# Kernel tuning notes

Measured on AMD Instinct MI355X. Metric: run time of the kernel, lower is better.

The kernel has to match this reference:

```python
import jax, jax.numpy as jnp
import numpy as np

DIM = 4096
N_HEADS = 32
HEAD_DIM = 128
N_KV = 8
REP = N_HEADS // N_KV  # 4
B = 8       # number of packed sequences (block-diagonal blocks)
S = 1024    # tokens per sequence
T = B * S   # seqlen_sum = 8192


def setup_inputs() -> dict:
    key = jax.random.key(0)
    ks = jax.random.split(key, 6)
    x = jax.random.normal(ks[0], (T, DIM), dtype=jnp.float32)
    # RoPE freqs: positions restart at 0 for each packed sequence
    pos = jnp.tile(jnp.arange(S, dtype=jnp.float32), B)            # [T]
    inv_freq = 1.0 / (10000.0 ** (jnp.arange(0, HEAD_DIM, 2, dtype=jnp.float32) / HEAD_DIM))  # [HEAD_DIM//2]
    freqs = pos[:, None] * inv_freq[None, :]                       # [T, HEAD_DIM//2]
    cos = jnp.cos(freqs)
    sin = jnp.sin(freqs)
    s = 0.02
    wq = jax.random.normal(ks[1], (DIM, N_HEADS * HEAD_DIM), dtype=jnp.float32) * s
    wk = jax.random.normal(ks[2], (DIM, N_KV * HEAD_DIM), dtype=jnp.float32) * s
    wv = jax.random.normal(ks[3], (DIM, N_KV * HEAD_DIM), dtype=jnp.float32) * s
    wo = jax.random.normal(ks[4], (N_HEADS * HEAD_DIM, DIM), dtype=jnp.float32) * s
    return {"x": x, "cos": cos, "sin": sin, "wq": wq, "wk": wk, "wv": wv, "wo": wo}


def _rope(t, cos, sin):
    # t: [T, H, D]; cos/sin: [T, D//2]; complex rotation on (even, odd) pairs
    th, hd = t.shape[1], t.shape[2]
    tp = t.reshape(t.shape[0], th, hd // 2, 2)
    te, to = tp[..., 0], tp[..., 1]
    c = cos[:, None, :]
    s = sin[:, None, :]
    oe = te * c - to * s
    oo = te * s + to * c
    return jnp.stack([oe, oo], axis=-1).reshape(t.shape)


def reference(x, cos, sin, wq, wk, wv, wo):
    scale = HEAD_DIM ** -0.5
    q = (x @ wq).reshape(T, N_HEADS, HEAD_DIM)
    k = (x @ wk).reshape(T, N_KV, HEAD_DIM)
    v = (x @ wv).reshape(T, N_KV, HEAD_DIM)
    q = _rope(q, cos, sin)
    k = _rope(k, cos, sin)
    # Block-diagonal mask with equal blocks == batched attention over B sequences.
    # GQA: q head index h = kv*REP + r (matches repeat_interleave on kv dim),
    # so group q heads as [N_KV, REP] instead of materializing repeated K/V.
    q = q.reshape(B, S, N_KV, REP, HEAD_DIM)
    k = k.reshape(B, S, N_KV, HEAD_DIM)
    v = v.reshape(B, S, N_KV, HEAD_DIM)
    scores = jnp.einsum('bqkrd,bskd->bkrqs', q, k) * scale   # [B, N_KV, REP, S, S]
    attn = jax.nn.softmax(scores, axis=-1)
    out = jnp.einsum('bkrqs,bskd->bqkrd', attn, v)           # [B, S, N_KV, REP, D]
    out = out.reshape(T, N_HEADS * HEAD_DIM)
    return out @ wo
```

## Files before the change

kernel.cpp:

```cpp
#include <hip/hip_runtime.h>
#include <math.h>

typedef unsigned short ushort_t;
typedef __attribute__((ext_vector_type(8))) short short8;
typedef __attribute__((ext_vector_type(4))) float f32x4;

#define MFMA16(a, b, c) __builtin_amdgcn_mfma_f32_16x16x32_bf16(a, b, c, 0, 0, 0)

__device__ __forceinline__ ushort_t f2bf(float f) {
    union { float f; unsigned u; } v;
    v.f = f;
    unsigned r = v.u + 0x7FFF + ((v.u >> 16) & 1);
    return (ushort_t)(r >> 16);
}

__device__ __forceinline__ void gload_lds16(const ushort_t* g, ushort_t* l) {
    __builtin_amdgcn_global_load_lds(
        (const __attribute__((address_space(1))) void*)g,
        (__attribute__((address_space(3))) void*)l, 16, 0, 0);
}

__global__ __launch_bounds__(256) void cast_f32_bf16(const float* __restrict__ src,
                                                     ushort_t* __restrict__ dst, int n8) {
    int i = blockIdx.x * 256 + threadIdx.x;
    if (i >= n8) return;
    const float4* s = (const float4*)src;
    float4 a = s[2 * i], b = s[2 * i + 1];
    union { ushort_t u[8]; uint4 v; } o;
    o.u[0] = f2bf(a.x); o.u[1] = f2bf(a.y); o.u[2] = f2bf(a.z); o.u[3] = f2bf(a.w);
    o.u[4] = f2bf(b.x); o.u[5] = f2bf(b.y); o.u[6] = f2bf(b.z); o.u[7] = f2bf(b.w);
    ((uint4*)dst)[i] = o.v;
}

__global__ __launch_bounds__(256) void transpose_cast(const float* __restrict__ src,
                                                      int D, int N,
                                                      ushort_t* __restrict__ dst, int dstStride) {
    __shared__ float t[32][33];
    int n0 = blockIdx.x * 32, d0 = blockIdx.y * 32;
    int tx = threadIdx.x & 31, ty = threadIdx.x >> 5;
#pragma unroll
    for (int i = 0; i < 4; i++)
        t[ty + 8 * i][tx] = src[(size_t)(d0 + ty + 8 * i) * N + n0 + tx];
    __syncthreads();
#pragma unroll
    for (int i = 0; i < 4; i++) {
        int n = ty + 8 * i;
        dst[(size_t)(n0 + n) * dstStride + d0 + tx] = f2bf(t[tx][n]);
    }
}

__global__ __launch_bounds__(256) void transpose_v(const ushort_t* __restrict__ qkv,
                                                   ushort_t* __restrict__ vt) {
    __shared__ ushort_t t[32][33];
    int bk = blockIdx.z; int b = bk >> 3, kvh = bk & 7;
    int s0 = blockIdx.x * 32, d0 = blockIdx.y * 32;
    int tx = threadIdx.x & 31, ty = threadIdx.x >> 5;
#pragma unroll
    for (int i = 0; i < 4; i++)
        t[ty + 8 * i][tx] = qkv[(size_t)(b * 1024 + s0 + ty + 8 * i) * 6144 + 5120 + kvh * 128 + d0 + tx];
    __syncthreads();
#pragma unroll
    for (int i = 0; i < 4; i++)
        vt[((size_t)(b * 8 + kvh) * 128 + d0 + ty + 8 * i) * 1024 + s0 + tx] = t[tx][ty + 8 * i];
}

template <int EPI>
__global__ __launch_bounds__(512, 2) void gemm8x(
    const ushort_t* __restrict__ A, const ushort_t* __restrict__ Bt,
    ushort_t* __restrict__ obf, float* __restrict__ of32,
    int M, int N, int K,
    const float* __restrict__ cosT, const float* __restrict__ sinT) {
    extern __shared__ __align__(16) ushort_t lds[];
    const int tid = threadIdx.x;
    const int lane = tid & 63, wv = tid >> 6;
    const int wr = wv >> 2, wc = wv & 3;
    const int lr = lane & 15, g = lane >> 4;

    const int gx = gridDim.x;
    const int nwg = gx * gridDim.y;
    const int bid = blockIdx.y * gx + blockIdx.x;
    const int swz = (bid & 7) * (nwg >> 3) + (bid >> 3);
    const int brow = (swz / gx) * 256, bcol = (swz % gx) * 256;

    const int st_r = tid >> 3, st_p = tid & 7;
    const int cA = (st_p ^ (st_r & 7)) * 8;
    const size_t aS0 = (size_t)(brow + st_r) * K + cA;
    const size_t bS0 = (size_t)(bcol + st_r) * K + cA;
    const int dstT = st_r * 64 + st_p * 8;

    const int sl0 = (g ^ (lr & 7)) * 8;
    const int sl1 = ((4 + g) ^ (lr & 7)) * 8;
    const int aRow = (wr * 128 + lr) * 64;
    const int bRow = (wc * 64 + lr) * 64;

    f32x4 acc[8][4];
#pragma unroll
    for (int m = 0; m < 8; m++)
#pragma unroll
        for (int n = 0; n < 4; n++) acc[m][n] = (f32x4){0.f, 0.f, 0.f, 0.f};

#define STG_A(kn, roff)                                                          \
    gload_lds16(A + aS0 + (size_t)(roff) * K + (size_t)(kn) * 64,                \
                lds + ((kn) & 1) * 16384 + (roff) * 64 + dstT)
#define STG_B(kn, roff)                                                          \
    gload_lds16(Bt + bS0 + (size_t)(roff) * K + (size_t)(kn) * 64,               \
                lds + 32768 + ((kn) & 1) * 16384 + (roff) * 64 + dstT)

    STG_B(0, 0);  STG_B(0, 64);
    STG_B(0, 128); STG_B(0, 192);
    STG_A(0, 0);  STG_A(0, 128);
    STG_A(0, 64); STG_A(0, 192);

    const int NKT = K >> 6;
    for (int kt = 0; kt < NKT; ++kt) {
        const int buf = (kt & 1) * 16384;
        const bool stg = kt < NKT - 1;
        const int kn = kt + 1;
        short8 bfr[4], af[4];

        asm volatile("s_waitcnt vmcnt(2)" ::: "memory");
        __builtin_amdgcn_s_barrier();
        __builtin_amdgcn_sched_barrier(0);
#pragma unroll
        for (int n = 0; n < 4; ++n)
            bfr[n] = *(const short8*)(lds + 32768 + buf + bRow + n * 1024 + sl0);
#pragma unroll
        for (int m = 0; m < 4; ++m)
            af[m] = *(const short8*)(lds + buf + aRow + m * 1024 + sl0);
        if (stg) { STG_B(kn, 0); STG_B(kn, 64); }
        __builtin_amdgcn_sched_barrier(0);
        __builtin_amdgcn_s_setprio(1);
#pragma unroll
        for (int m = 0; m < 4; ++m)
#pragma unroll
            for (int n = 0; n < 4; ++n)
                acc[m][n] = MFMA16(af[m], bfr[n], acc[m][n]);
        __builtin_amdgcn_s_setprio(0);

        if (kt == NKT - 1) asm volatile("s_waitcnt vmcnt(0)" ::: "memory");
        else               asm volatile("s_waitcnt vmcnt(2)" ::: "memory");
        __builtin_amdgcn_s_barrier();
        __builtin_amdgcn_sched_barrier(0);
#pragma unroll
        for (int m = 0; m < 4; ++m)
            af[m] = *(const short8*)(lds + buf + aRow + 4096 + m * 1024 + sl0);
        if (stg) { STG_B(kn, 128); STG_B(kn, 192); }
        __builtin_amdgcn_sched_barrier(0);
        __builtin_amdgcn_s_setprio(1);
#pragma unroll
        for (int m = 0; m < 4; ++m)
#pragma unroll
            for (int n = 0; n < 4; ++n)
                acc[m + 4][n] = MFMA16(af[m], bfr[n], acc[m + 4][n]);
        __builtin_amdgcn_s_setprio(0);

        __builtin_amdgcn_s_barrier();
        __builtin_amdgcn_sched_barrier(0);
#pragma unroll
        for (int n = 0; n < 4; ++n)
            bfr[n] = *(const short8*)(lds + 32768 + buf + bRow + n * 1024 + sl1);
#pragma unroll
        for (int m = 0; m < 4; ++m)
            af[m] = *(const short8*)(lds + buf + aRow + m * 1024 + sl1);
        if (stg) { STG_A(kn, 0); STG_A(kn, 128); }
        __builtin_amdgcn_sched_barrier(0);
        __builtin_amdgcn_s_setprio(1);
#pragma unroll
        for (int m = 0; m < 4; ++m)
#pragma unroll
            for (int n = 0; n < 4; ++n)
                acc[m][n] = MFMA16(af[m], bfr[n], acc[m][n]);
        __builtin_amdgcn_s_setprio(0);

        __builtin_amdgcn_s_barrier();
        __builtin_amdgcn_sched_barrier(0);
#pragma unroll
        for (int m = 0; m < 4; ++m)
            af[m] = *(const short8*)(lds + buf + aRow + 4096 + m * 1024 + sl1);
        if (stg) { STG_A(kn, 64); STG_A(kn, 192); }
        __builtin_amdgcn_sched_barrier(0);
        __builtin_amdgcn_s_setprio(1);
#pragma unroll
        for (int m = 0; m < 4; ++m)
#pragma unroll
            for (int n = 0; n < 4; ++n)
                acc[m + 4][n] = MFMA16(af[m], bfr[n], acc[m + 4][n]);
        __builtin_amdgcn_s_setprio(0);
    }
#undef STG_A
#undef STG_B

#pragma unroll
    for (int m = 0; m < 8; ++m) {
#pragma unroll
        for (int n = 0; n < 4; ++n) {
#pragma unroll
            for (int reg = 0; reg < 4; ++reg) {
                int r = brow + wr * 128 + m * 16 + g * 4 + reg;
                int c = bcol + wc * 64 + n * 16 + lr;
                float val = acc[m][n][reg];
                if (EPI == 1) {
                    float other = __shfl_xor(val, 1, 64);
                    if (c < 5120) {
                        int pos = r & 1023;
                        int pair = (c & 127) >> 1;
                        float cz = cosT[pos * 64 + pair];
                        float sz = sinT[pos * 64 + pair];
                        val = val * cz + other * ((c & 1) ? sz : -sz);
                        if (c < 4096) val *= 0.12752551286084110f;
                    }
                    obf[(size_t)r * N + c] = f2bf(val);
                } else {
                    of32[(size_t)r * N + c] = val;
                }
            }
        }
    }
}

__global__ __launch_bounds__(512, 2) void attn_fwd2(const ushort_t* __restrict__ qkv,
                                                    const ushort_t* __restrict__ vt,
                                                    ushort_t* __restrict__ aout) {
    extern __shared__ __align__(16) ushort_t lds[];
    const int tid = threadIdx.x, lane = tid & 63, w = tid >> 6;
    const int lr = lane & 15, g = lane >> 4;
    const int hr = w & 3, qc = w >> 2;
    const int qt = blockIdx.x, kvh = blockIdx.y, b = blockIdx.z;
    const int h = kvh * 4 + hr;
    const size_t qRow0 = (size_t)b * 1024 + qt * 64 + qc * 32;
    const size_t kBase = (size_t)b * 1024 * 6144 + 4096 + kvh * 128;
    const size_t vBase = (size_t)(b * 8 + kvh) * 128 * 1024;
    ushort_t* Pw = lds + 32768 + w * 2304;

    short8 qf[2][4];
#pragma unroll
    for (int qg = 0; qg < 2; ++qg)
#pragma unroll
        for (int kd = 0; kd < 4; ++kd)
            qf[qg][kd] = *(const short8*)&qkv[(qRow0 + qg * 16 + lr) * 6144 + h * 128 + kd * 32 + g * 8];

    f32x4 o[2][8];
#pragma unroll
    for (int qg = 0; qg < 2; ++qg)
#pragma unroll
        for (int nd = 0; nd < 8; ++nd) o[qg][nd] = (f32x4){0.f, 0.f, 0.f, 0.f};
    f32x4 lsum[2];
    lsum[0] = (f32x4){0.f, 0.f, 0.f, 0.f};
    lsum[1] = (f32x4){0.f, 0.f, 0.f, 0.f};

#define STAGE_KV(kt)                                                                   \
    {                                                                                  \
        const int buf_ = (kt) & 1;                                                     \
        {                                                                              \
            const int r0_ = tid >> 4, p_ = tid & 15;                                   \
            gload_lds16(qkv + kBase + (size_t)((kt) * 64 + r0_) * 6144 + ((p_ ^ (r0_ & 7)) * 8), \
                        lds + buf_ * 8192 + r0_ * 128 + p_ * 8);                       \
            const int r1_ = r0_ + 32;                                                  \
            gload_lds16(qkv + kBase + (size_t)((kt) * 64 + r1_) * 6144 + ((p_ ^ (r1_ & 7)) * 8), \
                        lds + buf_ * 8192 + r1_ * 128 + p_ * 8);                       \
        }                                                                              \
        {                                                                              \
            const int d0_ = tid >> 3, p_ = tid & 7;                                    \
            gload_lds16(vt + vBase + (size_t)d0_ * 1024 + (kt) * 64 + ((p_ ^ (d0_ & 7)) * 8), \
                        lds + 16384 + buf_ * 8192 + d0_ * 64 + p_ * 8);                \
            const int d1_ = d0_ + 64;                                                  \
            gload_lds16(vt + vBase + (size_t)d1_ * 1024 + (kt) * 64 + ((p_ ^ (d1_ & 7)) * 8), \
                        lds + 16384 + buf_ * 8192 + d1_ * 64 + p_ * 8);                \
        }                                                                              \
    }

    STAGE_KV(0);

    for (int kt = 0; kt < 16; ++kt) {
        const int buf = kt & 1;
        if (kt < 15) {
            STAGE_KV(kt + 1);
            asm volatile("s_waitcnt vmcnt(4)" ::: "memory");
        } else {
            asm volatile("s_waitcnt vmcnt(0)" ::: "memory");
        }
        __builtin_amdgcn_s_barrier();

        f32x4 sc[2][4];
#pragma unroll
        for (int qg = 0; qg < 2; ++qg)
#pragma unroll
            for (int ns = 0; ns < 4; ++ns) sc[qg][ns] = (f32x4){0.f, 0.f, 0.f, 0.f};
        __builtin_amdgcn_s_setprio(1);
#pragma unroll
        for (int ns = 0; ns < 4; ++ns) {
            const int key = ns * 16 + lr;
#pragma unroll
            for (int kd = 0; kd < 4; ++kd) {
                const short8 kf = *(const short8*)(lds + buf * 8192 + key * 128 +
                                                   (((kd * 4 + g) ^ (lr & 7)) * 8));
                sc[0][ns] = MFMA16(qf[0][kd], kf, sc[0][ns]);
                sc[1][ns] = MFMA16(qf[1][kd], kf, sc[1][ns]);
            }
        }
        __builtin_amdgcn_s_setprio(0);

#pragma unroll
        for (int qg = 0; qg < 2; ++qg) {
#pragma unroll
            for (int ns = 0; ns < 4; ++ns) {
#pragma unroll
                for (int j = 0; j < 4; ++j) {
                    float p = exp2f(sc[qg][ns][j]);
                    sc[qg][ns][j] = p;
                    lsum[qg][j] += p;
                }
            }
        }
#pragma unroll
        for (int qg = 0; qg < 2; ++qg)
#pragma unroll
            for (int ns = 0; ns < 4; ++ns)
#pragma unroll
                for (int j = 0; j < 4; ++j)
                    Pw[(qg * 16 + g * 4 + j) * 72 + ns * 16 + lr] = f2bf(sc[qg][ns][j]);

        __builtin_amdgcn_s_setprio(1);
#pragma unroll
        for (int ks = 0; ks < 2; ++ks) {
            short8 pa[2];
            pa[0] = *(const short8*)(Pw + (0 + lr) * 72 + ks * 32 + g * 8);
            pa[1] = *(const short8*)(Pw + (16 + lr) * 72 + ks * 32 + g * 8);
#pragma unroll
            for (int nd = 0; nd < 8; ++nd) {
                const int d = nd * 16 + lr;
                const short8 vf = *(const short8*)(lds + 16384 + buf * 8192 + d * 64 +
                                                   (((ks * 4 + g) ^ (d & 7)) * 8));
                o[0][nd] = MFMA16(pa[0], vf, o[0][nd]);
                o[1][nd] = MFMA16(pa[1], vf, o[1][nd]);
            }
        }
        __builtin_amdgcn_s_setprio(0);
        __builtin_amdgcn_s_barrier();
    }
#undef STAGE_KV

#pragma unroll
    for (int qg = 0; qg < 2; ++qg) {
#pragma unroll
        for (int j = 0; j < 4; ++j) {
            float s = lsum[qg][j];
            s += __shfl_xor(s, 1, 64);
            s += __shfl_xor(s, 2, 64);
            s += __shfl_xor(s, 4, 64);
            s += __shfl_xor(s, 8, 64);
            const float inv = 1.0f / s;
            const size_t r = qRow0 + qg * 16 + g * 4 + j;
#pragma unroll
            for (int nd = 0; nd < 8; ++nd)
                aout[r * 4096 + h * 128 + nd * 16 + lr] = f2bf(o[qg][nd][j] * inv);
        }
    }
}

extern "C" void kernel_launch(void* const* d_in, const int* in_sizes, int n_in,
                              void* d_out, int out_size, void* d_ws, size_t ws_size,
                              hipStream_t stream) {
    const float* x    = (const float*)d_in[0];
    const float* cosT = (const float*)d_in[1];
    const float* sinT = (const float*)d_in[2];
    const float* wq   = (const float*)d_in[3];
    const float* wk   = (const float*)d_in[4];
    const float* wv   = (const float*)d_in[5];
    const float* wo   = (const float*)d_in[6];
    float* out = (float*)d_out;

    char* ws = (char*)d_ws;
    ushort_t* xb   = (ushort_t*)(ws);
    ushort_t* wT   = (ushort_t*)(ws + 67108864);
    ushort_t* woT  = (ushort_t*)(ws + 117440512);
    ushort_t* qkv  = (ushort_t*)(ws + 150994944);
    ushort_t* vtb  = (ushort_t*)(ws + 67108864);
    ushort_t* attn = (ushort_t*)(ws);

    hipFuncSetAttribute((const void*)gemm8x<1>, hipFuncAttributeMaxDynamicSharedMemorySize, 131072);
    hipFuncSetAttribute((const void*)gemm8x<2>, hipFuncAttributeMaxDynamicSharedMemorySize, 131072);
    hipFuncSetAttribute((const void*)attn_fwd2, hipFuncAttributeMaxDynamicSharedMemorySize, 102400);

    cast_f32_bf16<<<16384, 256, 0, stream>>>(x, xb, 8192 * 4096 / 8);
    transpose_cast<<<dim3(128, 128), 256, 0, stream>>>(wq, 4096, 4096, wT, 4096);
    transpose_cast<<<dim3(32, 128), 256, 0, stream>>>(wk, 4096, 1024, wT + (size_t)4096 * 4096, 4096);
    transpose_cast<<<dim3(32, 128), 256, 0, stream>>>(wv, 4096, 1024, wT + (size_t)5120 * 4096, 4096);
    transpose_cast<<<dim3(128, 128), 256, 0, stream>>>(wo, 4096, 4096, woT, 4096);

    gemm8x<1><<<dim3(24, 32), 512, 131072, stream>>>(xb, wT, qkv, nullptr, 8192, 6144, 4096, cosT, sinT);
    transpose_v<<<dim3(32, 4, 64), 256, 0, stream>>>(qkv, vtb);
    attn_fwd2<<<dim3(16, 8, 8), 512, 102400, stream>>>(qkv, vtb, attn);
    gemm8x<2><<<dim3(16, 32), 512, 131072, stream>>>(attn, woT, nullptr, out, 8192, 4096, 4096, nullptr, nullptr);
}
```

Measured before the change: 940.8 us.

## Triple-buffer A tiles in GEMM LDS pipeline with two-stage-ahead prefetch

Restructures the bf16 GEMM main loop so A tiles are triple-buffered in LDS and prefetched two K-steps ahead, while B stays double-buffered. Waits and barriers are reorganized: a single vmcnt wait per iteration, explicit lgkmcnt waits before each MFMA block, and extra barriers around each LDS read phase. The aim is to hide more global-load latency behind MFMA work. In exchange, dynamic LDS grows to 160KB, which fills the whole LDS per CU, and the added barriers could add synchronization stalls.

```diff
diff --git a/kernel.cpp b/kernel.cpp
--- a/kernel.cpp
+++ b/kernel.cpp
@@ -65,7 +65,7 @@
 }
 
 template <int EPI>
-__global__ __launch_bounds__(512, 2) void gemm8x(
+__global__ __launch_bounds__(512, 2) void gemm9(
     const ushort_t* __restrict__ A, const ushort_t* __restrict__ Bt,
     ushort_t* __restrict__ obf, float* __restrict__ of32,
     int M, int N, int K,
@@ -101,33 +101,34 @@
 
 #define STG_A(kn, roff)                                                          \
     gload_lds16(A + aS0 + (size_t)(roff) * K + (size_t)(kn) * 64,                \
-                lds + ((kn) & 1) * 16384 + (roff) * 64 + dstT)
+                lds + ((kn) % 3) * 16384 + (roff) * 64 + dstT)
 #define STG_B(kn, roff)                                                          \
     gload_lds16(Bt + bS0 + (size_t)(roff) * K + (size_t)(kn) * 64,               \
-                lds + 32768 + ((kn) & 1) * 16384 + (roff) * 64 + dstT)
-
-    STG_B(0, 0);  STG_B(0, 64);
-    STG_B(0, 128); STG_B(0, 192);
-    STG_A(0, 0);  STG_A(0, 128);
-    STG_A(0, 64); STG_A(0, 192);
+                lds + 49152 + ((kn) & 1) * 16384 + (roff) * 64 + dstT)
+
+    STG_A(0, 0); STG_A(0, 64); STG_A(0, 128); STG_A(0, 192);
+    STG_B(0, 0); STG_B(0, 64); STG_B(0, 128); STG_B(0, 192);
+    STG_A(1, 0); STG_A(1, 64); STG_A(1, 128); STG_A(1, 192);
+    asm volatile("s_waitcnt vmcnt(4)" ::: "memory");
+    __builtin_amdgcn_s_barrier();
 
     const int NKT = K >> 6;
     for (int kt = 0; kt < NKT; ++kt) {
-        const int buf = (kt & 1) * 16384;
-        const bool stg = kt < NKT - 1;
-        const int kn = kt + 1;
+        const int sa = (kt % 3) * 16384;
+        const int sb = 49152 + (kt & 1) * 16384;
+        const bool stgB = kt < NKT - 1;
+        const bool stgA = kt < NKT - 2;
         short8 bfr[4], af[4];
 
-        asm volatile("s_waitcnt vmcnt(2)" ::: "memory");
-        __builtin_amdgcn_s_barrier();
-        __builtin_amdgcn_sched_barrier(0);
 #pragma unroll
         for (int n = 0; n < 4; ++n)
-            bfr[n] = *(const short8*)(lds + 32768 + buf + bRow + n * 1024 + sl0);
-#pragma unroll
-        for (int m = 0; m < 4; ++m)
-            af[m] = *(const short8*)(lds + buf + aRow + m * 1024 + sl0);
-        if (stg) { STG_B(kn, 0); STG_B(kn, 64); }
+            bfr[n] = *(const short8*)(lds + sb + bRow + n * 1024 + sl0);
+#pragma unroll
+        for (int m = 0; m < 4; ++m)
+            af[m] = *(const short8*)(lds + sa + aRow + m * 1024 + sl0);
+        if (stgB) { STG_B(kt + 1, 0); STG_B(kt + 1, 64); }
+        __builtin_amdgcn_s_barrier();
+        asm volatile("s_waitcnt lgkmcnt(0)" ::: "memory");
         __builtin_amdgcn_sched_barrier(0);
         __builtin_amdgcn_s_setprio(1);
 #pragma unroll
@@ -136,15 +137,14 @@
             for (int n = 0; n < 4; ++n)
                 acc[m][n] = MFMA16(af[m], bfr[n], acc[m][n]);
         __builtin_amdgcn_s_setprio(0);
-
-        if (kt == NKT - 1) asm volatile("s_waitcnt vmcnt(0)" ::: "memory");
-        else               asm volatile("s_waitcnt vmcnt(2)" ::: "memory");
-        __builtin_amdgcn_s_barrier();
-        __builtin_amdgcn_sched_barrier(0);
-#pragma unroll
-        for (int m = 0; m < 4; ++m)
-            af[m] = *(const short8*)(lds + buf + aRow + 4096 + m * 1024 + sl0);
-        if (stg) { STG_B(kn, 128); STG_B(kn, 192); }
+        __builtin_amdgcn_s_barrier();
+
+#pragma unroll
+        for (int m = 0; m < 4; ++m)
+            af[m] = *(const short8*)(lds + sa + aRow + 4096 + m * 1024 + sl0);
+        if (stgB) { STG_B(kt + 1, 128); STG_B(kt + 1, 192); }
+        __builtin_amdgcn_s_barrier();
+        asm volatile("s_waitcnt lgkmcnt(0)" ::: "memory");
         __builtin_amdgcn_sched_barrier(0);
         __builtin_amdgcn_s_setprio(1);
 #pragma unroll
@@ -153,16 +153,17 @@
             for (int n = 0; n < 4; ++n)
                 acc[m + 4][n] = MFMA16(af[m], bfr[n], acc[m + 4][n]);
         __builtin_amdgcn_s_setprio(0);
-
-        __builtin_amdgcn_s_barrier();
-        __builtin_amdgcn_sched_barrier(0);
+        __builtin_amdgcn_s_barrier();
+
 #pragma unroll
         for (int n = 0; n < 4; ++n)
-            bfr[n] = *(const short8*)(lds + 32768 + buf + bRow + n * 1024 + sl1);
-#pragma unroll
-        for (int m = 0; m < 4; ++m)
-            af[m] = *(const short8*)(lds + buf + aRow + m * 1024 + sl1);
-        if (stg) { STG_A(kn, 0); STG_A(kn, 128); }
+            bfr[n] = *(const short8*)(lds + sb + bRow + n * 1024 + sl1);
+#pragma unroll
+        for (int m = 0; m < 4; ++m)
+            af[m] = *(const short8*)(lds + sa + aRow + m * 1024 + sl1);
+        if (stgA) { STG_A(kt + 2, 0); STG_A(kt + 2, 64); }
+        __builtin_amdgcn_s_barrier();
+        asm volatile("s_waitcnt lgkmcnt(0)" ::: "memory");
         __builtin_amdgcn_sched_barrier(0);
         __builtin_amdgcn_s_setprio(1);
 #pragma unroll
@@ -171,13 +172,16 @@
             for (int n = 0; n < 4; ++n)
                 acc[m][n] = MFMA16(af[m], bfr[n], acc[m][n]);
         __builtin_amdgcn_s_setprio(0);
-
-        __builtin_amdgcn_s_barrier();
-        __builtin_amdgcn_sched_barrier(0);
-#pragma unroll
-        for (int m = 0; m < 4; ++m)
-            af[m] = *(const short8*)(lds + buf + aRow + 4096 + m * 1024 + sl1);
-        if (stg) { STG_A(kn, 64); STG_A(kn, 192); }
+        __builtin_amdgcn_s_barrier();
+
+#pragma unroll
+        for (int m = 0; m < 4; ++m)
+            af[m] = *(const short8*)(lds + sa + aRow + 4096 + m * 1024 + sl1);
+        if (stgA) { STG_A(kt + 2, 128); STG_A(kt + 2, 192); }
+        if (kt < NKT - 2)       asm volatile("s_waitcnt vmcnt(4)" ::: "memory");
+        else if (kt == NKT - 2) asm volatile("s_waitcnt vmcnt(0)" ::: "memory");
+        __builtin_amdgcn_s_barrier();
+        asm volatile("s_waitcnt lgkmcnt(0)" ::: "memory");
         __builtin_amdgcn_sched_barrier(0);
         __builtin_amdgcn_s_setprio(1);
 #pragma unroll
@@ -186,6 +190,7 @@
             for (int n = 0; n < 4; ++n)
                 acc[m + 4][n] = MFMA16(af[m], bfr[n], acc[m + 4][n]);
         __builtin_amdgcn_s_setprio(0);
+        __builtin_amdgcn_s_barrier();
     }
 #undef STG_A
 #undef STG_B
@@ -378,8 +383,8 @@
     ushort_t* vtb  = (ushort_t*)(ws + 67108864);
     ushort_t* attn = (ushort_t*)(ws);
 
-    hipFuncSetAttribute((const void*)gemm8x<1>, hipFuncAttributeMaxDynamicSharedMemorySize, 131072);
-    hipFuncSetAttribute((const void*)gemm8x<2>, hipFuncAttributeMaxDynamicSharedMemorySize, 131072);
+    hipFuncSetAttribute((const void*)gemm9<1>, hipFuncAttributeMaxDynamicSharedMemorySize, 163840);
+    hipFuncSetAttribute((const void*)gemm9<2>, hipFuncAttributeMaxDynamicSharedMemorySize, 163840);
     hipFuncSetAttribute((const void*)attn_fwd2, hipFuncAttributeMaxDynamicSharedMemorySize, 102400);
 
     cast_f32_bf16<<<16384, 256, 0, stream>>>(x, xb, 8192 * 4096 / 8);
@@ -388,8 +393,8 @@
     transpose_cast<<<dim3(32, 128), 256, 0, stream>>>(wv, 4096, 1024, wT + (size_t)5120 * 4096, 4096);
     transpose_cast<<<dim3(128, 128), 256, 0, stream>>>(wo, 4096, 4096, woT, 4096);
 
-    gemm8x<1><<<dim3(24, 32), 512, 131072, stream>>>(xb, wT, qkv, nullptr, 8192, 6144, 4096, cosT, sinT);
+    gemm9<1><<<dim3(24, 32), 512, 163840, stream>>>(xb, wT, qkv, nullptr, 8192, 6144, 4096, cosT, sinT);
     transpose_v<<<dim3(32, 4, 64), 256, 0, stream>>>(qkv, vtb);
     attn_fwd2<<<dim3(16, 8, 8), 512, 102400, stream>>>(qkv, vtb, attn);
-    gemm8x<2><<<dim3(16, 32), 512, 131072, stream>>>(attn, woT, nullptr, out, 8192, 4096, 4096, nullptr, nullptr);
-}
+    gemm9<2><<<dim3(16, 32), 512, 163840, stream>>>(attn, woT, nullptr, out, 8192, 4096, 4096, nullptr, nullptr);
+}
```

Result: no change. 950.3 us (+1.0%).
